# Optimization experiments

Measured on AMD Instinct MI355X. Metric: run time of the kernel, lower is better.

## Reference

```python
import jax, jax.numpy as jnp
import numpy as np

B, S, D = 2, 2048, 1024
H, DH = 16, 64
IGNORE = -100000.0
ATTN_SCALE = float(np.sqrt(DH))


def setup_inputs() -> dict:
    key = jax.random.key(0)
    ks = jax.random.split(key, 9)
    sc = 0.02
    return {
        "x": jax.random.normal(ks[0], (B, S, D), dtype=jnp.float32),
        "W_Q": jax.random.normal(ks[1], (H, DH, D), dtype=jnp.float32) * sc,
        "W_K": jax.random.normal(ks[2], (H, DH, D), dtype=jnp.float32) * sc,
        "W_V": jax.random.normal(ks[3], (H, DH, D), dtype=jnp.float32) * sc,
        "W_O": jax.random.normal(ks[4], (H, D, DH), dtype=jnp.float32) * sc,
        "b_Q": jax.random.normal(ks[5], (H, DH), dtype=jnp.float32) * sc,
        "b_K": jax.random.normal(ks[6], (H, DH), dtype=jnp.float32) * sc,
        "b_V": jax.random.normal(ks[7], (H, DH), dtype=jnp.float32) * sc,
        "b_O": jax.random.normal(ks[8], (D,), dtype=jnp.float32) * sc,
    }


def reference(x, W_Q, W_K, W_V, W_O, b_Q, b_K, b_V, b_O):
    # QKV projections: [b, pos, head, d_head]
    q = jnp.einsum('ihm,bpm->bpih', W_Q, x) + b_Q
    k = jnp.einsum('ihm,bpm->bpih', W_K, x) + b_K
    v = jnp.einsum('ihm,bpm->bpih', W_V, x) + b_V
    # scores[b, head, query_pos, key_pos]
    scores = jnp.einsum('bpih,bqih->bipq', q, k) / ATTN_SCALE
    Sq = x.shape[1]
    causal = jnp.tril(jnp.ones((Sq, Sq), dtype=bool))  # global causal mask
    scores = jnp.where(causal, scores, jnp.float32(IGNORE))
    attn = jax.nn.softmax(scores, axis=-1)
    # z[b, query_pos, head, d_head]
    z = jnp.einsum('bpih,biqp->bqih', v, attn)
    out = jnp.einsum('idh,bqih->bqd', W_O, z) + b_O
    return out
```

## Files before the change

### kernel.cpp

```cpp
#include <hip/hip_runtime.h>
#include <stdint.h>

typedef __attribute__((ext_vector_type(8))) short short8;
typedef __attribute__((ext_vector_type(4))) float f32x4;

#define AS1(p) ((const __attribute__((address_space(1))) void*)(p))
#define AS3(p) ((__attribute__((address_space(3))) void*)(p))

__device__ __forceinline__ void gload_lds16(const void* g, void* l) {
  __builtin_amdgcn_global_load_lds(AS1(g), AS3(l), 16, 0, 0);
}

__device__ __forceinline__ uint32_t cvtpk_bf16(float a, float b) {
  uint32_t d;
  asm("v_cvt_pk_bf16_f32 %0, %1, %2" : "=v"(d) : "v"(a), "v"(b));
  return d;
}

__device__ __forceinline__ float fast_exp2(float x) {
#if __has_builtin(__builtin_amdgcn_exp2f)
  return __builtin_amdgcn_exp2f(x);
#else
  return exp2f(x);
#endif
}

#define QSCALE 0.1803368801111244f

__global__ void prep_k(const float* __restrict__ x, const float* __restrict__ wq,
                       const float* __restrict__ wk, const float* __restrict__ wv,
                       const float* __restrict__ wo, const float* __restrict__ bq,
                       const float* __restrict__ bk, const float* __restrict__ bv,
                       uint2* __restrict__ xb, uint2* __restrict__ wqkvb,
                       uint2* __restrict__ mob, float* __restrict__ bqkv) {
  const int bid = blockIdx.x, tid = threadIdx.x;
  if (bid < 4096) {
    int i = bid * 256 + tid;
    float4 v = ((const float4*)x)[i];
    uint2 o; o.x = cvtpk_bf16(v.x, v.y); o.y = cvtpk_bf16(v.z, v.w);
    xb[i] = o;
  } else if (bid < 7168) {
    int i = (bid - 4096) * 256 + tid;
    int e = i * 4;
    const float* src = (e < (1 << 20)) ? (wq + e)
                     : (e < (2 << 20)) ? (wk + (e - (1 << 20)))
                                       : (wv + (e - (2 << 20)));
    float4 v = *(const float4*)src;
    uint2 o; o.x = cvtpk_bf16(v.x, v.y); o.y = cvtpk_bf16(v.z, v.w);
    wqkvb[i] = o;
  } else if (bid < 8192) {
    int i = (bid - 7168) * 256 + tid;
    int o4 = i * 4;
    int d = o4 >> 10, c = o4 & 1023;
    const float* s = wo + ((c >> 6) << 16) + (d << 6) + (c & 63);
    float4 v = *(const float4*)s;
    uint2 o; o.x = cvtpk_bf16(v.x, v.y); o.y = cvtpk_bf16(v.z, v.w);
    mob[i] = o;
  } else {
    int i = (bid - 8192) * 256 + tid;
    bqkv[i] = (i < 1024) ? bq[i] : (i < 2048) ? bk[i - 1024] : bv[i - 2048];
  }
}

template <int EPI>
__global__ __launch_bounds__(256) void gemm_bt(const short* __restrict__ A,
                                               const short* __restrict__ Bm,
                                               const float* __restrict__ bias,
                                               void* __restrict__ Cout, int K, int ldc) {
  __shared__ short As[128 * 64];
  __shared__ short Bs[128 * 64];
  const int t = threadIdx.x;
  const int l = t & 63, w = t >> 6;
  const int wr = w >> 1, wc = w & 1;
  const int q = l & 15, g = l >> 4;
  const long brow = (long)blockIdx.y * 128;
  const long bcol = (long)blockIdx.x * 128;
  f32x4 acc[4][4] = {};
  const int r8 = t >> 3;
  const int sc8 = (t & 7) ^ (r8 & 7);
  const short* aptr = A + (brow + r8) * (long)K + sc8 * 8;
  const short* bptr = Bm + (bcol + r8) * (long)K + sc8 * 8;
  const int qs = q & 7;
  for (int k0 = 0; k0 < K; k0 += 64) {
#pragma unroll
    for (int c = 0; c < 4; ++c) {
      gload_lds16(aptr + k0 + c * 32 * (long)K, &As[(c * 256 + t) * 8]);
      gload_lds16(bptr + k0 + c * 32 * (long)K, &Bs[(c * 256 + t) * 8]);
    }
    __syncthreads();
    short8 af[4][2], bfr[4][2];
#pragma unroll
    for (int m = 0; m < 4; ++m)
#pragma unroll
      for (int kk = 0; kk < 2; ++kk)
        af[m][kk] = *(const short8*)&As[(wr * 64 + m * 16 + q) * 64 + ((kk * 4 + g) ^ qs) * 8];
#pragma unroll
    for (int n = 0; n < 4; ++n)
#pragma unroll
      for (int kk = 0; kk < 2; ++kk)
        bfr[n][kk] = *(const short8*)&Bs[(wc * 64 + n * 16 + q) * 64 + ((kk * 4 + g) ^ qs) * 8];
#pragma unroll
    for (int m = 0; m < 4; ++m)
#pragma unroll
      for (int n = 0; n < 4; ++n) {
        acc[m][n] = __builtin_amdgcn_mfma_f32_16x16x32_bf16(af[m][0], bfr[n][0], acc[m][n], 0, 0, 0);
        acc[m][n] = __builtin_amdgcn_mfma_f32_16x16x32_bf16(af[m][1], bfr[n][1], acc[m][n], 0, 0, 0);
      }
    if (k0 + 64 < K) __syncthreads();
  }
#pragma unroll
  for (int m = 0; m < 4; ++m)
#pragma unroll
    for (int n = 0; n < 4; ++n)
#pragma unroll
      for (int r = 0; r < 4; ++r) {
        long row = brow + wr * 64 + m * 16 + g * 4 + r;
        long col = bcol + wc * 64 + n * 16 + q;
        float v = acc[m][n][r] + bias[col];
        if (EPI == 0) {
          if (col < 1024) v *= QSCALE;
          ((unsigned short*)Cout)[row * ldc + col] = (unsigned short)cvtpk_bf16(v, v);
        } else {
          ((float*)Cout)[row * ldc + col] = v;
        }
      }
}

__global__ __launch_bounds__(256) void attn(const short* __restrict__ qkv,
                                            unsigned short* __restrict__ zb) {
  __shared__ short Ks[2][64 * 64];
  __shared__ short Vt[64 * 64];
  __shared__ unsigned short Ps[8][16 * 64];
  const int bid = blockIdx.x;
  const int r_ = bid >> 7;
  const int u_ = (bid >> 3) & 15;
  const int x_ = bid & 7;
  const int bh = r_ * 8 + x_;
  const int pi = (r_ < 2) ? u_ : 15 - u_;
  const int qtA = 2 * pi + 1, qtB = 2 * pi;
  const int b = bh >> 4, h = bh & 15;
  const int t = threadIdx.x, l = t & 63, w = t >> 6;
  const int lq = l & 15, g = l >> 4;
  const int u = t >> 3, c8 = t & 7;
  const long rowbase = (long)b * 2048;
  const short* qp = qkv + rowbase * 3072 + h * 64;
  const short* kp = qp + 1024;
  const short* vp = qp + 2048;

  short8 qfA[2], qfB[2];
#pragma unroll
  for (int kg = 0; kg < 2; ++kg) {
    qfA[kg] = *(const short8*)(qp + (long)(qtA * 64 + w * 16 + lq) * 3072 + kg * 32 + g * 8);
    qfB[kg] = *(const short8*)(qp + (long)(qtB * 64 + w * 16 + lq) * 3072 + kg * 32 + g * 8);
  }
  f32x4 zA[4] = {}, zB[4] = {};
  float mA = -1e30f, lA = 0.0f, mB = -1e30f, lB = 0.0f;

  auto step = [&](const short* ksb, unsigned short* Pw, f32x4 (&zacc)[4],
                  float& mrun, float& lrun, short8 (&qf)[2], bool diag) {
    f32x4 sacc[4] = {};
#pragma unroll
    for (int m = 0; m < 4; ++m) {
#pragma unroll
      for (int kg = 0; kg < 2; ++kg) {
        int krow = m * 16 + lq;
        int blk = kg * 4 + g;
        short8 kf = *(const short8*)&ksb[krow * 64 + (blk ^ (krow & 7)) * 8];
        sacc[m] = __builtin_amdgcn_mfma_f32_16x16x32_bf16(kf, qf[kg], sacc[m], 0, 0, 0);
      }
    }
    if (diag) {
#pragma unroll
      for (int m = 0; m < 4; ++m)
#pragma unroll
        for (int r = 0; r < 4; ++r)
          if (m * 16 + g * 4 + r > w * 16 + lq) sacc[m][r] = -1e30f;
    }
    float red[8];
#pragma unroll
    for (int i2 = 0; i2 < 8; ++i2)
      red[i2] = fmaxf(sacc[i2 >> 2][i2 & 3], sacc[2 + (i2 >> 2)][i2 & 3]);
#pragma unroll
    for (int i2 = 0; i2 < 4; ++i2) red[i2] = fmaxf(red[i2], red[i2 + 4]);
    float mx = fmaxf(fmaxf(red[0], red[2]), fmaxf(red[1], red[3]));
    mx = fmaxf(mx, __shfl_xor(mx, 16));
    mx = fmaxf(mx, __shfl_xor(mx, 32));
    if (!__all(mx <= mrun + 8.0f)) {
      float mnew = fmaxf(mrun, mx);
      float alpha = fast_exp2(mrun - mnew);
      lrun *= alpha;
#pragma unroll
      for (int r = 0; r < 4; ++r) {
        float ar = __shfl(alpha, g * 4 + r);
#pragma unroll
        for (int n2 = 0; n2 < 4; ++n2) zacc[n2][r] *= ar;
      }
      mrun = mnew;
    }
#pragma unroll
    for (int m = 0; m < 4; ++m)
#pragma unroll
      for (int r = 0; r < 4; ++r) sacc[m][r] = fast_exp2(sacc[m][r] - mrun);
    float rs[8];
#pragma unroll
    for (int i2 = 0; i2 < 8; ++i2)
      rs[i2] = sacc[i2 >> 2][i2 & 3] + sacc[2 + (i2 >> 2)][i2 & 3];
#pragma unroll
    for (int i2 = 0; i2 < 4; ++i2) rs[i2] = rs[i2] + rs[i2 + 4];
    float ts = (rs[0] + rs[2]) + (rs[1] + rs[3]);
    ts += __shfl_xor(ts, 16);
    ts += __shfl_xor(ts, 32);
    lrun += ts;
#pragma unroll
    for (int m = 0; m < 4; ++m) {
      uint2 wv;
      wv.x = cvtpk_bf16(sacc[m][0], sacc[m][1]);
      wv.y = cvtpk_bf16(sacc[m][2], sacc[m][3]);
      int c = m * 4 + g;
      int csw = c ^ ((lq & 7) << 1);
      *(uint2*)&Pw[lq * 64 + csw * 4] = wv;
    }
    short8 pf[2];
#pragma unroll
    for (int kg2 = 0; kg2 < 2; ++kg2) {
      int c0 = kg2 * 8 + g * 2;
      int c0s = c0 ^ ((lq & 7) << 1);
      pf[kg2] = *(const short8*)&Pw[lq * 64 + c0s * 4];
    }
#pragma unroll
    for (int n2 = 0; n2 < 4; ++n2) {
#pragma unroll
      for (int kg2 = 0; kg2 < 2; ++kg2) {
        int dh = n2 * 16 + lq;
        int sw = (dh & 7) ^ ((dh >> 3) & 7);
        int blk = kg2 * 4 + g;
        short8 vf = *(const short8*)&Vt[dh * 64 + ((blk ^ sw) * 8)];
        zacc[n2] = __builtin_amdgcn_mfma_f32_16x16x32_bf16(pf[kg2], vf, zacc[n2], 0, 0, 0);
      }
    }
  };

  auto stageK = [&](int tile, int buf) {
#pragma unroll
    for (int i = 0; i < 2; ++i) {
      int r = i * 32 + u;
      int cbk = (c8 ^ (r & 7)) * 8;
      gload_lds16(kp + (long)(tile * 64 + r) * 3072 + cbk, &Ks[buf][i * 2048 + t * 8]);
    }
  };

  short8 va0, va1;
  {
    stageK(0, 0);
    const short* vrow = vp + (long)(2 * u) * 3072 + c8 * 8;
    va0 = *(const short8*)vrow;
    va1 = *(const short8*)(vrow + 3072);
  }

  for (int j = 0; j <= qtA; ++j) {
    const int buf = j & 1;
    asm volatile("s_waitcnt vmcnt(0)" ::: "memory");
    __builtin_amdgcn_sched_barrier(0);
    __builtin_amdgcn_s_barrier();
    {
      int blk = u >> 2, rl = (u & 3) * 2;
#pragma unroll
      for (int idx = 0; idx < 8; ++idx) {
        int dh = c8 * 8 + idx;
        int sw = (dh & 7) ^ ((dh >> 3) & 7);
        uint32_t pk = (uint32_t)(uint16_t)va0[idx] | ((uint32_t)(uint16_t)va1[idx] << 16);
        *(uint32_t*)&Vt[dh * 64 + ((blk ^ sw) * 8) + rl] = pk;
      }
    }
    if (j < qtA) {
      stageK(j + 1, buf ^ 1);
      const short* vrow = vp + (long)((j + 1) * 64 + 2 * u) * 3072 + c8 * 8;
      va0 = *(const short8*)vrow;
      va1 = *(const short8*)(vrow + 3072);
    }
    asm volatile("s_waitcnt lgkmcnt(0)" ::: "memory");
    __builtin_amdgcn_sched_barrier(0);
    __builtin_amdgcn_s_barrier();
    step(&Ks[buf][0], &Ps[w][0], zA, mA, lA, qfA, j == qtA);
    if (j <= qtB)
      step(&Ks[buf][0], &Ps[4 + w][0], zB, mB, lB, qfB, j == qtB);
  }

  auto wout = [&](f32x4 (&zacc)[4], float lrun, int qt) {
#pragma unroll
    for (int r = 0; r < 4; ++r) {
      float linv = 1.0f / __shfl(lrun, g * 4 + r);
      long grow = rowbase + qt * 64 + w * 16 + g * 4 + r;
#pragma unroll
      for (int n2 = 0; n2 < 4; ++n2) {
        int col = h * 64 + n2 * 16 + lq;
        float zv = zacc[n2][r] * linv;
        zb[grow * 1024 + col] = (unsigned short)cvtpk_bf16(zv, zv);
      }
    }
  };
  wout(zA, lA, qtA);
  wout(zB, lB, qtB);
}

extern "C" void kernel_launch(void* const* d_in, const int* in_sizes, int n_in,
                              void* d_out, int out_size, void* d_ws, size_t ws_size,
                              hipStream_t stream) {
  const float* x  = (const float*)d_in[0];
  const float* wq = (const float*)d_in[1];
  const float* wk = (const float*)d_in[2];
  const float* wv = (const float*)d_in[3];
  const float* wo = (const float*)d_in[4];
  const float* bq = (const float*)d_in[5];
  const float* bk = (const float*)d_in[6];
  const float* bv = (const float*)d_in[7];
  const float* bo = (const float*)d_in[8];
  char* ws = (char*)d_ws;
  if (ws_size < ((size_t)48 * 1024 * 1024 + 16384)) return;
  short*          xb    = (short*)(ws);
  short*          qkvb  = (short*)(ws + ((size_t)8  << 20));
  unsigned short* zbuf  = (unsigned short*)(ws + ((size_t)32 << 20));
  short*          wqkvb = (short*)(ws + ((size_t)40 << 20));
  short*          mob   = (short*)(ws + ((size_t)46 << 20));
  float*          bqkv  = (float*)(ws + ((size_t)48 << 20));

  prep_k<<<8204, 256, 0, stream>>>(x, wq, wk, wv, wo, bq, bk, bv,
                                   (uint2*)xb, (uint2*)wqkvb, (uint2*)mob, bqkv);
  gemm_bt<0><<<dim3(24, 32), 256, 0, stream>>>(xb, wqkvb, bqkv, (void*)qkvb, 1024, 3072);
  attn      <<<512,          256, 0, stream>>>(qkvb, zbuf);
  gemm_bt<1><<<dim3(8, 32),  256, 0, stream>>>((const short*)zbuf, mob, bo, d_out, 1024, 1024);
}
```

Baseline: 121.3 us.

## Split attention blocks to one query tile each, doubling grid size

Each attention block previously handled two adjacent query tiles that shared the staged K/V tiles. It now handles a single query tile, and the grid doubles to 1024 blocks, with a reversed tile order on alternate rows to balance causal work. This halves LDS for P and the register state per block, which can raise occupancy and improve load balance on the many-CU GPU. In exchange, K/V tiles are loaded from global memory twice as often across blocks, since the cross-tile reuse is lost.

```diff
diff --git a/kernel.cpp b/kernel.cpp
--- a/kernel.cpp
+++ b/kernel.cpp
@@ -130,14 +130,13 @@
                                             unsigned short* __restrict__ zb) {
   __shared__ short Ks[2][64 * 64];
   __shared__ short Vt[64 * 64];
-  __shared__ unsigned short Ps[8][16 * 64];
+  __shared__ unsigned short Ps[4][16 * 64];
   const int bid = blockIdx.x;
-  const int r_ = bid >> 7;
-  const int u_ = (bid >> 3) & 15;
+  const int r_ = bid >> 8;
   const int x_ = bid & 7;
+  const int u_ = (bid >> 3) & 31;
   const int bh = r_ * 8 + x_;
-  const int pi = (r_ < 2) ? u_ : 15 - u_;
-  const int qtA = 2 * pi + 1, qtB = 2 * pi;
+  const int qt = (r_ & 1) ? u_ : 31 - u_;
   const int b = bh >> 4, h = bh & 15;
   const int t = threadIdx.x, l = t & 63, w = t >> 6;
   const int lq = l & 15, g = l >> 4;
@@ -147,17 +146,15 @@
   const short* kp = qp + 1024;
   const short* vp = qp + 2048;
 
-  short8 qfA[2], qfB[2];
-#pragma unroll
-  for (int kg = 0; kg < 2; ++kg) {
-    qfA[kg] = *(const short8*)(qp + (long)(qtA * 64 + w * 16 + lq) * 3072 + kg * 32 + g * 8);
-    qfB[kg] = *(const short8*)(qp + (long)(qtB * 64 + w * 16 + lq) * 3072 + kg * 32 + g * 8);
-  }
-  f32x4 zA[4] = {}, zB[4] = {};
-  float mA = -1e30f, lA = 0.0f, mB = -1e30f, lB = 0.0f;
-
-  auto step = [&](const short* ksb, unsigned short* Pw, f32x4 (&zacc)[4],
-                  float& mrun, float& lrun, short8 (&qf)[2], bool diag) {
+  short8 qf[2];
+#pragma unroll
+  for (int kg = 0; kg < 2; ++kg)
+    qf[kg] = *(const short8*)(qp + (long)(qt * 64 + w * 16 + lq) * 3072 + kg * 32 + g * 8);
+  f32x4 zacc[4] = {};
+  float mrun = -1e30f, lrun = 0.0f;
+  unsigned short* Pw = &Ps[w][0];
+
+  auto step = [&](const short* ksb, bool diag) {
     f32x4 sacc[4] = {};
 #pragma unroll
     for (int m = 0; m < 4; ++m) {
@@ -257,7 +254,7 @@
     va1 = *(const short8*)(vrow + 3072);
   }
 
-  for (int j = 0; j <= qtA; ++j) {
+  for (int j = 0; j <= qt; ++j) {
     const int buf = j & 1;
     asm volatile("s_waitcnt vmcnt(0)" ::: "memory");
     __builtin_amdgcn_sched_barrier(0);
@@ -272,7 +269,7 @@
         *(uint32_t*)&Vt[dh * 64 + ((blk ^ sw) * 8) + rl] = pk;
       }
     }
-    if (j < qtA) {
+    if (j < qt) {
       stageK(j + 1, buf ^ 1);
       const short* vrow = vp + (long)((j + 1) * 64 + 2 * u) * 3072 + c8 * 8;
       va0 = *(const short8*)vrow;
@@ -281,26 +278,20 @@
     asm volatile("s_waitcnt lgkmcnt(0)" ::: "memory");
     __builtin_amdgcn_sched_barrier(0);
     __builtin_amdgcn_s_barrier();
-    step(&Ks[buf][0], &Ps[w][0], zA, mA, lA, qfA, j == qtA);
-    if (j <= qtB)
-      step(&Ks[buf][0], &Ps[4 + w][0], zB, mB, lB, qfB, j == qtB);
-  }
-
-  auto wout = [&](f32x4 (&zacc)[4], float lrun, int qt) {
-#pragma unroll
-    for (int r = 0; r < 4; ++r) {
-      float linv = 1.0f / __shfl(lrun, g * 4 + r);
-      long grow = rowbase + qt * 64 + w * 16 + g * 4 + r;
-#pragma unroll
-      for (int n2 = 0; n2 < 4; ++n2) {
-        int col = h * 64 + n2 * 16 + lq;
-        float zv = zacc[n2][r] * linv;
-        zb[grow * 1024 + col] = (unsigned short)cvtpk_bf16(zv, zv);
-      }
-    }
-  };
-  wout(zA, lA, qtA);
-  wout(zB, lB, qtB);
+    step(&Ks[buf][0], j == qt);
+  }
+
+#pragma unroll
+  for (int r = 0; r < 4; ++r) {
+    float linv = 1.0f / __shfl(lrun, g * 4 + r);
+    long grow = rowbase + qt * 64 + w * 16 + g * 4 + r;
+#pragma unroll
+    for (int n2 = 0; n2 < 4; ++n2) {
+      int col = h * 64 + n2 * 16 + lq;
+      float zv = zacc[n2][r] * linv;
+      zb[grow * 1024 + col] = (unsigned short)cvtpk_bf16(zv, zv);
+    }
+  }
 }
 
 extern "C" void kernel_launch(void* const* d_in, const int* in_sizes, int n_in,
@@ -327,6 +318,6 @@
   prep_k<<<8204, 256, 0, stream>>>(x, wq, wk, wv, wo, bq, bk, bv,
                                    (uint2*)xb, (uint2*)wqkvb, (uint2*)mob, bqkv);
   gemm_bt<0><<<dim3(24, 32), 256, 0, stream>>>(xb, wqkvb, bqkv, (void*)qkvb, 1024, 3072);
-  attn      <<<512,          256, 0, stream>>>(qkvb, zbuf);
+  attn      <<<1024,         256, 0, stream>>>(qkvb, zbuf);
   gemm_bt<1><<<dim3(8, 32),  256, 0, stream>>>((const short*)zbuf, mob, bo, d_out, 1024, 1024);
 }
```

New measurement: 117.6 us. 1.03x faster.
